# Kernel tuning notes

Measured on AMD Instinct MI355X. Metric: run time of the kernel, lower is better.

## Reference

```python
import jax, jax.numpy as jnp
import numpy as np

NUM_HEADS = 12

def _pe(L, d):
    # standard sinusoidal positional encoding, shape (1, L, d)
    pos = jnp.arange(L, dtype=jnp.float32)[:, None]
    i = jnp.arange(d)[None, :]
    angle = pos / jnp.power(10000.0, (2 * (i // 2)).astype(jnp.float32) / d)
    pe = jnp.where(i % 2 == 0, jnp.sin(angle), jnp.cos(angle))
    return pe[None]

def _ln(x, scale, bias, eps=1e-5):
    m = x.mean(-1, keepdims=True)
    v = ((x - m) ** 2).mean(-1, keepdims=True)
    return (x - m) / jnp.sqrt(v + eps) * scale + bias

def setup_inputs() -> dict:
    key = jax.random.key(0)
    ks = jax.random.split(key, 8)
    D = 768
    s = 0.02
    return {
        "x": jax.random.normal(ks[0], (8, D, 32, 32), jnp.float32),
        "context_token": jax.random.normal(ks[1], (1, 1, D), jnp.float32),
        "register_tokens": jax.random.normal(ks[2], (1, 4, D), jnp.float32),
        "in_proj_w": jax.random.normal(ks[3], (3 * D, D), jnp.float32) * s,
        "in_proj_b": jnp.zeros((3 * D,), jnp.float32),
        "out_proj_w": jax.random.normal(ks[4], (D, D), jnp.float32) * s,
        "out_proj_b": jnp.zeros((D,), jnp.float32),
        "ln1_s": jnp.ones((D,), jnp.float32),
        "ln1_b": jnp.zeros((D,), jnp.float32),
        "ln2_s": jnp.ones((D,), jnp.float32),
        "ln2_b": jnp.zeros((D,), jnp.float32),
        "ffn_w1": jax.random.normal(ks[5], (4 * D, D), jnp.float32) * s,
        "ffn_b1": jnp.zeros((4 * D,), jnp.float32),
        "ffn_w2": jax.random.normal(ks[6], (D, 4 * D), jnp.float32) * s,
        "ffn_b2": jnp.zeros((D,), jnp.float32),
    }

def reference(x, context_token, register_tokens, in_proj_w, in_proj_b,
              out_proj_w, out_proj_b, ln1_s, ln1_b, ln2_s, ln2_b,
              ffn_w1, ffn_b1, ffn_w2, ffn_b2):
    B, d, h, w = x.shape
    N = h * w
    R = register_tokens.shape[1]
    G = 1 + R  # global tokens: context + registers
    nh = NUM_HEADS
    dh = d // nh
    # (B, N, d)
    x_flat = x.reshape(B, d, N).transpose(0, 2, 1)
    tokens = jnp.concatenate([
        jnp.broadcast_to(context_token, (B, 1, d)),
        jnp.broadcast_to(register_tokens, (B, R, d)),
    ], axis=1)
    tokens = tokens + _pe(G, d)
    xwt = _ln(jnp.concatenate([tokens, x_flat], axis=1), ln1_s, ln1_b)
    S = G + N
    # MultiheadAttention (eval mode, dropout off): fused in-projection
    qkv = xwt @ in_proj_w.T + in_proj_b
    q, k, v = jnp.split(qkv, 3, axis=-1)
    to_heads = lambda t: t.reshape(B, S, nh, dh).transpose(0, 2, 1, 3)
    q, k, v = to_heads(q), to_heads(k), to_heads(v)
    scores = jnp.einsum('bhqd,bhkd->bhqk', q, k) / np.float32(np.sqrt(dh))
    # mask (True = disallowed): feature rows (>=G) cannot attend to global cols (<G);
    # global rows attend everything; feature-feature block allowed.
    row_feat = jnp.arange(S) >= G
    col_glob = jnp.arange(S) < G
    disallowed = row_feat[:, None] & col_glob[None, :]
    scores = jnp.where(disallowed, -jnp.inf, scores)
    attn = jax.nn.softmax(scores, axis=-1)
    o = jnp.einsum('bhqk,bhkd->bhqd', attn, v).transpose(0, 2, 1, 3).reshape(B, S, d)
    o = o @ out_proj_w.T + out_proj_b
    y = o + xwt
    ff = jax.nn.gelu(_ln(y, ln2_s, ln2_b) @ ffn_w1.T + ffn_b1, approximate=False) @ ffn_w2.T + ffn_b2
    y = y + ff
    context_out = y[:, 0:1, :]
    register_out = y[:, 1:G, :]
    feature_out = y[:, G:, :].transpose(0, 2, 1).reshape(B, d, h, w)
    return feature_out, context_out, register_out
```

## Files before the change

### kernel.cpp

```cpp
#include <hip/hip_runtime.h>
#include <hip/hip_bf16.h>
#include <cmath>

typedef unsigned short u16;
typedef __bf16 bf16x8 __attribute__((ext_vector_type(8)));
typedef float floatx4 __attribute__((ext_vector_type(4)));

#define SQ 1029
#define DM 768
#define NH 12
#define SQP 1088
#define SSC 0.18033688011112042f

#define GLD16(gp, lp) __builtin_amdgcn_global_load_lds( \
    (const __attribute__((address_space(1))) unsigned int*)(gp), \
    (__attribute__((address_space(3))) unsigned int*)(lp), 16, 0, 0)

#define OFF_WQKV ((size_t)0)
#define OFF_WOUT ((size_t)3538944)
#define OFF_W1   ((size_t)4718592)
#define OFF_W2   ((size_t)9437184)
#define OFF_XF   ((size_t)14155776)
#define OFF_XWT  ((size_t)26800128)
#define OFF_QKV  ((size_t)39444480)
#define OFF_VT   ((size_t)77783040)
#define OFF_Y    ((size_t)91152384)
#define OFF_BQ   ((size_t)103796736)

__device__ __forceinline__ float bf2f(u16 u) {
  unsigned int x = ((unsigned int)u) << 16;
  float f; __builtin_memcpy(&f, &x, 4); return f;
}
__device__ __forceinline__ u16 f2bf(float f) {
  unsigned int x; __builtin_memcpy(&x, &f, 4);
  x = (x + 0x7fffu + ((x >> 16) & 1u)) >> 16;
  return (u16)x;
}
__device__ __forceinline__ unsigned int pk_bf16(float a, float b) {
  __hip_bfloat162 h = __float22bfloat162_rn(make_float2(a, b));
  unsigned int u; __builtin_memcpy(&u, &h, 4); return u;
}

__device__ __forceinline__ void blockReduce2(float& s1, float& s2) {
  #pragma unroll
  for (int o = 32; o > 0; o >>= 1) { s1 += __shfl_xor(s1, o); s2 += __shfl_xor(s2, o); }
  __shared__ float t1[4], t2[4];
  const int w = threadIdx.x >> 6;
  if ((threadIdx.x & 63) == 0) { t1[w] = s1; t2[w] = s2; }
  __syncthreads();
  s1 = t1[0] + t1[1] + t1[2] + t1[3];
  s2 = t2[0] + t2[1] + t2[2] + t2[3];
}

__global__ __launch_bounds__(256) void convw_all(
    const float* __restrict__ a, const float* __restrict__ b,
    const float* __restrict__ c, const float* __restrict__ d,
    const float* __restrict__ bq, u16* __restrict__ dst, float* __restrict__ bqs) {
  int i = blockIdx.x * 256 + threadIdx.x;
  if (i >= 1770048) return;
  if (i >= 1769472) {
    const int off = i - 1769472;
    float4 v = ((const float4*)bq)[off];
    if (off < 192) { v.x *= SSC; v.y *= SSC; v.z *= SSC; v.w *= SSC; }
    ((float4*)bqs)[off] = v;
    return;
  }
  const float* src; int off;
  if (i < 442368)       { src = a; off = i; }
  else if (i < 589824)  { src = b; off = i - 442368; }
  else if (i < 1179648) { src = c; off = i - 589824; }
  else                  { src = d; off = i - 1179648; }
  float4 v = ((const float4*)src)[off];
  if (i < 147456) { v.x *= SSC; v.y *= SSC; v.z *= SSC; v.w *= SSC; }
  ushort4 o; o.x = f2bf(v.x); o.y = f2bf(v.y); o.z = f2bf(v.z); o.w = f2bf(v.w);
  ((ushort4*)dst)[i] = o;
}

__global__ __launch_bounds__(256) void ln1_fused(
    const float* __restrict__ x, const float* __restrict__ ctx, const float* __restrict__ regt,
    const float* __restrict__ g, const float* __restrict__ be, u16* __restrict__ xwt) {
  const int bx = blockIdx.x;
  const int tid = threadIdx.x;
  if (bx >= 256) {
    const int row = bx - 256;
    const int b = row / 5, s = row % 5;
    float v[3];
    #pragma unroll
    for (int i = 0; i < 3; ++i) {
      const int c = tid + i * 256;
      float tok = (s == 0) ? ctx[c] : regt[(s - 1) * DM + c];
      float e = (float)(2 * (c / 2)) * (1.0f / 768.0f);
      float ang = (float)s / powf(10000.0f, e);
      v[i] = tok + ((c & 1) ? cosf(ang) : sinf(ang));
    }
    float s1 = v[0] + v[1] + v[2];
    float s2 = v[0] * v[0] + v[1] * v[1] + v[2] * v[2];
    blockReduce2(s1, s2);
    const float mean = s1 * (1.0f / 768.0f);
    const float var = s2 * (1.0f / 768.0f) - mean * mean;
    const float rs = rsqrtf(fmaxf(var, 0.0f) + 1e-5f);
    #pragma unroll
    for (int i = 0; i < 3; ++i) {
      const int c = tid + i * 256;
      xwt[((size_t)b * SQ + s) * DM + c] = f2bf((v[i] - mean) * rs * g[c] + be[c]);
    }
    return;
  }
  __shared__ u16 XT[32][772];
  const int b = bx >> 5, st = bx & 31;
  const int i2 = tid & 15, cj = tid >> 4;
  const int n0 = st * 32;
  #pragma unroll 4
  for (int ct = 0; ct < 48; ++ct) {
    const int c = ct * 16 + cj;
    const float2 v = *(const float2*)&x[((size_t)b * 768 + c) * 1024 + n0 + i2 * 2];
    XT[i2 * 2][c]     = f2bf(v.x);
    XT[i2 * 2 + 1][c] = f2bf(v.y);
  }
  __syncthreads();
  const int wave = tid >> 6, lane = tid & 63;
  float gr[12], br[12];
  #pragma unroll
  for (int k = 0; k < 12; ++k) { gr[k] = g[lane + k * 64]; br[k] = be[lane + k * 64]; }
  #pragma unroll
  for (int rr = 0; rr < 8; ++rr) {
    const int row = wave * 8 + rr;
    float v[12];
    float s1 = 0.f, s2 = 0.f;
    #pragma unroll
    for (int k = 0; k < 12; ++k) {
      v[k] = bf2f(XT[row][lane + k * 64]);
      s1 += v[k]; s2 += v[k] * v[k];
    }
    #pragma unroll
    for (int o = 32; o > 0; o >>= 1) { s1 += __shfl_xor(s1, o); s2 += __shfl_xor(s2, o); }
    const float mean = s1 * (1.0f / 768.0f);
    const float var = s2 * (1.0f / 768.0f) - mean * mean;
    const float rs = rsqrtf(fmaxf(var, 0.0f) + 1e-5f);
    u16* dst = xwt + ((size_t)b * SQ + 5 + n0 + row) * DM;
    #pragma unroll
    for (int k = 0; k < 12; ++k)
      dst[lane + k * 64] = f2bf((v[k] - mean) * rs * gr[k] + br[k]);
  }
}

__global__ __launch_bounds__(256) void ln2k(
    const u16* __restrict__ y, const float* __restrict__ g, const float* __restrict__ be,
    u16* __restrict__ out) {
  const int row = blockIdx.x * 4 + (threadIdx.x >> 6);
  const int lane = threadIdx.x & 63;
  const u16* src = y + (size_t)row * DM;
  float v[12];
  float s1 = 0.f, s2 = 0.f;
  #pragma unroll
  for (int k = 0; k < 3; ++k) {
    const ushort4 u = *(const ushort4*)&src[k * 256 + lane * 4];
    const float a0 = bf2f(u.x), a1 = bf2f(u.y), a2 = bf2f(u.z), a3 = bf2f(u.w);
    v[k * 4 + 0] = a0; v[k * 4 + 1] = a1; v[k * 4 + 2] = a2; v[k * 4 + 3] = a3;
    s1 += (a0 + a1) + (a2 + a3);
    s2 += (a0 * a0 + a1 * a1) + (a2 * a2 + a3 * a3);
  }
  #pragma unroll
  for (int o = 32; o > 0; o >>= 1) { s1 += __shfl_xor(s1, o); s2 += __shfl_xor(s2, o); }
  const float mean = s1 * (1.0f / 768.0f);
  const float var = s2 * (1.0f / 768.0f) - mean * mean;
  const float rs = rsqrtf(fmaxf(var, 0.0f) + 1e-5f);
  u16* dst = out + (size_t)row * DM;
  #pragma unroll
  for (int k = 0; k < 3; ++k) {
    const float4 g4 = *(const float4*)&g[k * 256 + lane * 4];
    const float4 b4 = *(const float4*)&be[k * 256 + lane * 4];
    uint2 w;
    w.x = pk_bf16((v[k * 4 + 0] - mean) * rs * g4.x + b4.x,
                  (v[k * 4 + 1] - mean) * rs * g4.y + b4.y);
    w.y = pk_bf16((v[k * 4 + 2] - mean) * rs * g4.z + b4.z,
                  (v[k * 4 + 3] - mean) * rs * g4.w + b4.w);
    *(uint2*)&dst[k * 256 + lane * 4] = w;
  }
}

template<int EPI, int K, int NB>
__global__ __launch_bounds__(256) void gemmk(
    const u16* __restrict__ A, const u16* __restrict__ W, const float* __restrict__ bias,
    const u16* __restrict__ res, u16* __restrict__ out, int M) {
  constexpr int N = NB * 128;
  __shared__ u16 SM[16384];
  u16* Asm = SM;
  u16* Bsm = SM + 8192;
  const int tid = threadIdx.x, wave = tid >> 6, lane = tid & 63, quad = lane >> 4, l16 = lane & 15;
  const int lin = blockIdx.x;
  constexpr int FULL = 64 * NB;
  int mb, nb;
  if (lin < FULL) { const int g = lin / (8 * NB); const int r = lin - g * 8 * NB; mb = g * 8 + (r & 7); nb = r >> 3; }
  else { mb = 64; nb = lin - FULL; }
  const int m0 = mb * 128, n0 = nb * 128;
  const int wm = wave & 1, wn = wave >> 1;

  const u16* Ap[4]; const u16* Wp[4]; u16* la[4]; u16* lb[4];
  #pragma unroll
  for (int it = 0; it < 4; ++it) {
    const int c = it * 256 + tid;
    const int row = c >> 3, gch = (c & 7) ^ (row & 7);
    Ap[it] = A + (size_t)min(m0 + row, M - 1) * K + gch * 8;
    Wp[it] = W + (size_t)(n0 + row) * K + gch * 8;
    la[it] = Asm + c * 8;
    lb[it] = Bsm + c * 8;
  }

  floatx4 acc[4][4];
  #pragma unroll
  for (int i = 0; i < 4; ++i)
    #pragma unroll
    for (int j = 0; j < 4; ++j) { floatx4 z = {0.f, 0.f, 0.f, 0.f}; acc[i][j] = z; }

  const int ch0 = (quad ^ (l16 & 7)) << 3;
  const int ch1 = ((4 + quad) ^ (l16 & 7)) << 3;

  #pragma unroll 1
  for (int ko = 0; ko < K / 768; ++ko) {
    #pragma unroll
    for (int ki = 0; ki < 768; ki += 64) {
      __syncthreads();
      #pragma unroll
      for (int it = 0; it < 4; ++it) GLD16(Ap[it] + ki, la[it]);
      #pragma unroll
      for (int it = 0; it < 4; ++it) GLD16(Wp[it] + ki, lb[it]);
      __syncthreads();
      #pragma unroll
      for (int kk = 0; kk < 2; ++kk) {
        const int ch = kk ? ch1 : ch0;
        bf16x8 a[4], b[4];
        #pragma unroll
        for (int i = 0; i < 4; ++i) a[i] = *(const bf16x8*)&Asm[(wm * 64 + i * 16 + l16) * 64 + ch];
        #pragma unroll
        for (int j = 0; j < 4; ++j) b[j] = *(const bf16x8*)&Bsm[(wn * 64 + j * 16 + l16) * 64 + ch];
        #pragma unroll
        for (int i = 0; i < 4; ++i)
          #pragma unroll
          for (int j = 0; j < 4; ++j)
            acc[i][j] = __builtin_amdgcn_mfma_f32_16x16x32_bf16(b[j], a[i], acc[i][j], 0, 0, 0);
      }
    }
    if (K > 768) {
      #pragma unroll
      for (int it = 0; it < 4; ++it) { Ap[it] += 768; Wp[it] += 768; }
    }
  }

  #pragma unroll
  for (int j = 0; j < 4; ++j) {
    const float4 b4 = *(const float4*)(bias + n0 + wn * 64 + j * 16 + quad * 4);
    #pragma unroll
    for (int i = 0; i < 4; ++i) {
      acc[i][j][0] += b4.x; acc[i][j][1] += b4.y; acc[i][j][2] += b4.z; acc[i][j][3] += b4.w;
    }
  }
  if constexpr (EPI == 2) {
    #pragma unroll
    for (int i = 0; i < 4; ++i)
      #pragma unroll
      for (int j = 0; j < 4; ++j)
        #pragma unroll
        for (int r = 0; r < 4; ++r) {
          const float v = acc[i][j][r];
          acc[i][j][r] = v / (1.0f + exp2f(-2.3022221f * (v + 0.044715f * v * v * v)));
        }
  }
  __syncthreads();
  u16* Ep = SM + wave * 2304;
  #pragma unroll
  for (int h = 0; h < 2; ++h) {
    #pragma unroll
    for (int i2 = 0; i2 < 2; ++i2) {
      const int i = h * 2 + i2;
      #pragma unroll
      for (int j = 0; j < 4; ++j) {
        uint2 w;
        w.x = pk_bf16(acc[i][j][0], acc[i][j][1]);
        w.y = pk_bf16(acc[i][j][2], acc[i][j][3]);
        *(uint2*)&Ep[(i2 * 16 + l16) * 72 + j * 16 + quad * 4] = w;
      }
    }
    #pragma unroll
    for (int s = 0; s < 4; ++s) {
      const int lrow = s * 8 + (lane >> 3);
      const int gm = m0 + wm * 64 + h * 32 + lrow;
      const int gn = n0 + wn * 64 + (lane & 7) * 8;
      uint4 lv = *(const uint4*)&Ep[lrow * 72 + (lane & 7) * 8];
      if constexpr (EPI == 1 || EPI == 3) {
        const uint4 rv = *(const uint4*)(res + (size_t)min(gm, M - 1) * N + gn);
        const unsigned* lp = &lv.x; const unsigned* rp = &rv.x;
        uint4 ov; unsigned* op = &ov.x;
        #pragma unroll
        for (int d = 0; d < 4; ++d) {
          const float a0 = bf2f((u16)(lp[d] & 0xffffu)) + bf2f((u16)(rp[d] & 0xffffu));
          const float a1 = bf2f((u16)(lp[d] >> 16)) + bf2f((u16)(rp[d] >> 16));
          op[d] = pk_bf16(a0, a1);
        }
        lv = ov;
      }
      if (gm < M) *(uint4*)(out + (size_t)gm * N + gn) = lv;
    }
  }
}

template<int EPI, int K, int NB>
__global__ __launch_bounds__(128, 2) void gemmw(
    const u16* __restrict__ A, const u16* __restrict__ W, const float* __restrict__ bias,
    const u16* __restrict__ res, u16* __restrict__ out, int M) {
  constexpr int N = NB * 128;
  __shared__ u16 SM[16384];
  u16* Asm = SM;
  u16* Bsm = SM + 8192;
  const int tid = threadIdx.x, wave = tid >> 6, lane = tid & 63, quad = lane >> 4, l16 = lane & 15;
  const int lin = blockIdx.x;
  constexpr int FULL = 64 * NB;
  int mb, nb;
  if (lin < FULL) { const int g = lin / (8 * NB); const int r = lin - g * 8 * NB; mb = g * 8 + (r & 7); nb = r >> 3; }
  else { mb = 64; nb = lin - FULL; }
  const int m0 = mb * 128, n0 = nb * 128;

  const u16* Ap[8]; const u16* Wp[8];
  #pragma unroll
  for (int it = 0; it < 8; ++it) {
    const int row = it * 16 + (tid >> 3);
    const int gch = (tid & 7) ^ (row & 7);
    Ap[it] = A + (size_t)min(m0 + row, M - 1) * K + gch * 8;
    Wp[it] = W + (size_t)(n0 + row) * K + gch * 8;
  }

  floatx4 acc[8][4];
  #pragma unroll
  for (int i = 0; i < 8; ++i)
    #pragma unroll
    for (int j = 0; j < 4; ++j) { floatx4 z = {0.f, 0.f, 0.f, 0.f}; acc[i][j] = z; }

  const int ch0 = (quad ^ (l16 & 7)) << 3;
  const int ch1 = ((4 + quad) ^ (l16 & 7)) << 3;

  #pragma unroll 1
  for (int ko = 0; ko < K / 768; ++ko) {
    #pragma unroll
    for (int ki = 0; ki < 768; ki += 64) {
      __syncthreads();
      #pragma unroll
      for (int it = 0; it < 8; ++it) GLD16(Ap[it] + ki, (char*)SM + (it * 128 + tid) * 16);
      #pragma unroll
      for (int it = 0; it < 8; ++it) GLD16(Wp[it] + ki, (char*)SM + 16384 + (it * 128 + tid) * 16);
      __syncthreads();
      #pragma unroll
      for (int kk = 0; kk < 2; ++kk) {
        const int ch = kk ? ch1 : ch0;
        bf16x8 a[8], b[4];
        #pragma unroll
        for (int i = 0; i < 8; ++i) a[i] = *(const bf16x8*)&Asm[(i * 16 + l16) * 64 + ch];
        #pragma unroll
        for (int j = 0; j < 4; ++j) b[j] = *(const bf16x8*)&Bsm[(wave * 64 + j * 16 + l16) * 64 + ch];
        #pragma unroll
        for (int i = 0; i < 8; ++i)
          #pragma unroll
          for (int j = 0; j < 4; ++j)
            acc[i][j] = __builtin_amdgcn_mfma_f32_16x16x32_bf16(b[j], a[i], acc[i][j], 0, 0, 0);
      }
    }
    if (K > 768) {
      #pragma unroll
      for (int it = 0; it < 8; ++it) { Ap[it] += 768; Wp[it] += 768; }
    }
  }

  #pragma unroll
  for (int j = 0; j < 4; ++j) {
    const float4 b4 = *(const float4*)(bias + n0 + wave * 64 + j * 16 + quad * 4);
    #pragma unroll
    for (int i = 0; i < 8; ++i) {
      acc[i][j][0] += b4.x; acc[i][j][1] += b4.y; acc[i][j][2] += b4.z; acc[i][j][3] += b4.w;
    }
  }
  if constexpr (EPI == 2) {
    #pragma unroll
    for (int i = 0; i < 8; ++i)
      #pragma unroll
      for (int j = 0; j < 4; ++j)
        #pragma unroll
        for (int r = 0; r < 4; ++r) {
          const float v = acc[i][j][r];
          acc[i][j][r] = v / (1.0f + exp2f(-2.3022221f * (v + 0.044715f * v * v * v)));
        }
  }
  __syncthreads();
  u16* Ep = SM + wave * 2304;
  #pragma unroll
  for (int g = 0; g < 4; ++g) {
    #pragma unroll
    for (int i2 = 0; i2 < 2; ++i2) {
      const int i = g * 2 + i2;
      #pragma unroll
      for (int j = 0; j < 4; ++j) {
        uint2 w;
        w.x = pk_bf16(acc[i][j][0], acc[i][j][1]);
        w.y = pk_bf16(acc[i][j][2], acc[i][j][3]);
        *(uint2*)&Ep[(i2 * 16 + l16) * 72 + j * 16 + quad * 4] = w;
      }
    }
    #pragma unroll
    for (int s = 0; s < 4; ++s) {
      const int lrow = s * 8 + (lane >> 3);
      const int gm = m0 + g * 32 + lrow;
      const int gn = n0 + wave * 64 + (lane & 7) * 8;
      uint4 lv = *(const uint4*)&Ep[lrow * 72 + (lane & 7) * 8];
      if constexpr (EPI == 1 || EPI == 3) {
        const uint4 rv = *(const uint4*)(res + (size_t)min(gm, M - 1) * N + gn);
        const unsigned* lp = &lv.x; const unsigned* rp = &rv.x;
        uint4 ov; unsigned* op = &ov.x;
        #pragma unroll
        for (int d = 0; d < 4; ++d) {
          const float a0 = bf2f((u16)(lp[d] & 0xffffu)) + bf2f((u16)(rp[d] & 0xffffu));
          const float a1 = bf2f((u16)(lp[d] >> 16)) + bf2f((u16)(rp[d] >> 16));
          op[d] = pk_bf16(a0, a1);
        }
        lv = ov;
      }
      if (gm < M) *(uint4*)(out + (size_t)gm * N + gn) = lv;
    }
  }
}

__global__ __launch_bounds__(256) void vtrans(const u16* __restrict__ qkv, u16* __restrict__ vt) {
  __shared__ u16 t[32][33];
  const int bh = blockIdx.x, st = blockIdx.y, dt = blockIdx.z;
  const int bq = bh / NH, hh = bh % NH;
  u16* vd = vt + (size_t)bh * 64 * SQP;
  const int i = threadIdx.x, jj = threadIdx.y;
  #pragma unroll
  for (int kk = 0; kk < 4; ++kk) {
    int j = jj + kk * 8;
    t[j][i] = qkv[(size_t)(bq * SQ + st * 32 + j) * 2304 + 1536 + hh * 64 + dt * 32 + i];
  }
  __syncthreads();
  #pragma unroll
  for (int kk = 0; kk < 4; ++kk) {
    int j = jj + kk * 8;
    vd[(size_t)(dt * 32 + j) * SQP + st * 32 + i] = t[i][j];
  }
}

__global__ __launch_bounds__(256) void attn_flash(
    const u16* __restrict__ qkv, const u16* __restrict__ vt, u16* __restrict__ out) {
  const int bh = blockIdx.x, qt = blockIdx.y;
  const int b = bh / NH, h = bh % NH;
  const int tid = threadIdx.x, wave = tid >> 6, lane = tid & 63, quad = lane >> 4, l16 = lane & 15;
  __shared__ u16 Ks[4096], VTs[4096];
  __shared__ u16 Ps[64 * 72];
  const int q0 = qt * 64;
  const u16* qk = qkv + (size_t)b * SQ * 2304 + h * 64;
  const u16* vslab = vt + (size_t)bh * 64 * SQP;
  const int r0 = tid >> 3,         q0c = (tid & 7) ^ (r0 & 7);
  const int r1 = (tid + 256) >> 3, q1c = (tid & 7) ^ (r1 & 7);
  u16* L0K = Ks + wave * 512;  u16* L1K = Ks + 2048 + wave * 512;
  u16* L0V = VTs + wave * 512; u16* L1V = VTs + 2048 + wave * 512;

  const int qrow = wave * 16 + l16;
  const bf16x8 qf0 = *(const bf16x8*)&qk[(size_t)(q0 + qrow) * 2304 + quad * 8];
  const bf16x8 qf1 = *(const bf16x8*)&qk[(size_t)(q0 + qrow) * 2304 + (4 + quad) * 8];

  floatx4 Oa[4];
  #pragma unroll
  for (int nt = 0; nt < 4; ++nt) { floatx4 z = {0.f, 0.f, 0.f, 0.f}; Oa[nt] = z; }
  float l_acc = 0.f;
  const bool qfeat = (q0 + qrow >= 5);

  for (int t = 0; t < 17; ++t) {
    const int k0 = t * 64;
    __syncthreads();
    GLD16(qk + 768 + (size_t)(k0 + r0) * 2304 + q0c * 8, L0K);
    GLD16(qk + 768 + (size_t)(k0 + r1) * 2304 + q1c * 8, L1K);
    GLD16(vslab + (size_t)r0 * SQP + k0 + q0c * 8, L0V);
    GLD16(vslab + (size_t)r1 * SQP + k0 + q1c * 8, L1V);
    __syncthreads();

    floatx4 st[4];
    #pragma unroll
    for (int mt = 0; mt < 4; ++mt) { floatx4 z = {0.f, 0.f, 0.f, 0.f}; st[mt] = z; }
    #pragma unroll
    for (int kk = 0; kk < 2; ++kk) {
      const bf16x8 qf = kk ? qf1 : qf0;
      #pragma unroll
      for (int mt = 0; mt < 4; ++mt) {
        const int krow = mt * 16 + l16;
        bf16x8 kf = *(const bf16x8*)&Ks[krow * 64 + (((kk * 4 + quad) ^ (krow & 7)) << 3)];
        st[mt] = __builtin_amdgcn_mfma_f32_16x16x32_bf16(kf, qf, st[mt], 0, 0, 0);
      }
    }

    if (t == 16) {
      float p[4];
      #pragma unroll
      for (int r = 0; r < 4; ++r) {
        float pv = exp2f(st[0][r]);
        p[r] = (quad * 4 + r < 5) ? pv : 0.f;
      }
      l_acc += (p[0] + p[1]) + (p[2] + p[3]);
      uint2 w;
      w.x = pk_bf16(p[0], p[1]);
      w.y = pk_bf16(p[2], p[3]);
      *(uint2*)&Ps[qrow * 72 + quad * 4] = w;
      const uint2 zz = {0u, 0u};
      #pragma unroll
      for (int mt = 1; mt < 4; ++mt) *(uint2*)&Ps[qrow * 72 + mt * 16 + quad * 4] = zz;
    } else if (t == 0) {
      #pragma unroll
      for (int mt = 0; mt < 4; ++mt) {
        float p[4];
        #pragma unroll
        for (int r = 0; r < 4; ++r) {
          float pv = exp2f(st[mt][r]);
          if (mt == 0) pv = (qfeat && (quad * 4 + r < 5)) ? 0.f : pv;
          p[r] = pv;
        }
        l_acc += (p[0] + p[1]) + (p[2] + p[3]);
        uint2 w;
        w.x = pk_bf16(p[0], p[1]);
        w.y = pk_bf16(p[2], p[3]);
        *(uint2*)&Ps[qrow * 72 + mt * 16 + quad * 4] = w;
      }
    } else {
      #pragma unroll
      for (int mt = 0; mt < 4; ++mt) {
        float p[4];
        #pragma unroll
        for (int r = 0; r < 4; ++r) p[r] = exp2f(st[mt][r]);
        l_acc += (p[0] + p[1]) + (p[2] + p[3]);
        uint2 w;
        w.x = pk_bf16(p[0], p[1]);
        w.y = pk_bf16(p[2], p[3]);
        *(uint2*)&Ps[qrow * 72 + mt * 16 + quad * 4] = w;
      }
    }

    auto pv_step = [&](int kk) {
      bf16x8 pf = *(const bf16x8*)&Ps[qrow * 72 + kk * 32 + quad * 8];
      #pragma unroll
      for (int nt = 0; nt < 4; ++nt) {
        const int brow = nt * 16 + l16;
        bf16x8 bb = *(const bf16x8*)&VTs[brow * 64 + (((kk * 4 + quad) ^ (brow & 7)) << 3)];
        Oa[nt] = __builtin_amdgcn_mfma_f32_16x16x32_bf16(pf, bb, Oa[nt], 0, 0, 0);
      }
    };
    pv_step(0);
    if (t != 16) pv_step(1);
  }

  float lt = l_acc;
  lt += __shfl_xor(lt, 16);
  lt += __shfl_xor(lt, 32);
  lt = fmaxf(lt, 1e-30f);
  #pragma unroll
  for (int nt = 0; nt < 4; ++nt)
    #pragma unroll
    for (int r = 0; r < 4; ++r) {
      const int qo = quad * 4 + r;
      const float lr = __shfl(lt, (lane & 48) | qo);
      const int qg2 = q0 + wave * 16 + qo;
      if (qg2 < SQ)
        out[((size_t)b * SQ + qg2) * DM + h * 64 + nt * 16 + l16] = f2bf(Oa[nt][r] / lr);
    }
}

__global__ __launch_bounds__(256) void transpose_out(const u16* __restrict__ yf, float* __restrict__ out) {
  const int bx = blockIdx.x;
  const int tid = threadIdx.x;
  if (bx >= 6144) {
    const int idx = (bx - 6144) * 256 + tid;
    if (idx >= 8 * 5 * DM) return;
    const int b = idx / (5 * DM);
    const int r = idx % (5 * DM);
    const int s = r / DM, c = r % DM;
    const float v = bf2f(yf[((size_t)b * SQ + s) * DM + c]);
    if (s == 0) out[(size_t)6291456 + (size_t)b * DM + c] = v;
    else out[(size_t)6291456 + 6144 + ((size_t)b * 4 + (s - 1)) * DM + c] = v;
    return;
  }
  __shared__ u16 tile[32][33];
  const int b = bx / 768, rr = bx % 768, nt = rr / 24, ct = rr % 24;
  const int i = tid & 31, jj = tid >> 5;
  #pragma unroll
  for (int kk = 0; kk < 4; ++kk) {
    int j = jj + kk * 8;
    tile[j][i] = yf[((size_t)b * SQ + 5 + nt * 32 + j) * DM + ct * 32 + i];
  }
  __syncthreads();
  #pragma unroll
  for (int kk = 0; kk < 4; ++kk) {
    int j = jj + kk * 8;
    out[((size_t)b * 768 + ct * 32 + j) * 1024 + nt * 32 + i] = bf2f(tile[i][j]);
  }
}

extern "C" void kernel_launch(void* const* d_in, const int* in_sizes, int n_in,
                              void* d_out, int out_size, void* d_ws, size_t ws_size,
                              hipStream_t stream) {
  const float* x    = (const float*)d_in[0];
  const float* ctx  = (const float*)d_in[1];
  const float* regt = (const float*)d_in[2];
  const float* wqkv = (const float*)d_in[3];
  const float* bqkv = (const float*)d_in[4];
  const float* wout = (const float*)d_in[5];
  const float* bout = (const float*)d_in[6];
  const float* ln1s = (const float*)d_in[7];
  const float* ln1b = (const float*)d_in[8];
  const float* ln2s = (const float*)d_in[9];
  const float* ln2b = (const float*)d_in[10];
  const float* w1   = (const float*)d_in[11];
  const float* b1   = (const float*)d_in[12];
  const float* w2   = (const float*)d_in[13];
  const float* b2   = (const float*)d_in[14];

  char* ws = (char*)d_ws;
  u16* wb_all = (u16*)(ws + OFF_WQKV);
  u16* wqkv_b = (u16*)(ws + OFF_WQKV);
  u16* wout_b = (u16*)(ws + OFF_WOUT);
  u16* w1_b   = (u16*)(ws + OFF_W1);
  u16* w2_b   = (u16*)(ws + OFF_W2);
  u16* xwt    = (u16*)(ws + OFF_XWT);
  u16* qkv    = (u16*)(ws + OFF_QKV);
  u16* vtb    = (u16*)(ws + OFF_VT);
  u16* yb     = (u16*)(ws + OFF_Y);
  float* bqs  = (float*)(ws + OFF_BQ);
  u16* attnb  = (u16*)(ws + OFF_XF);
  u16* ynorm  = (u16*)(ws + OFF_XF);
  u16* h1     = (u16*)(ws + OFF_QKV);
  u16* yfin   = (u16*)(ws + OFF_XWT);
  float* outp = (float*)d_out;

  convw_all   <<<6915, 256, 0, stream>>>(wqkv, wout, w1, w2, bqkv, wb_all, bqs);
  ln1_fused   <<<296, 256, 0, stream>>>(x, ctx, regt, ln1s, ln1b, xwt);
  gemmw<0, 768, 18><<<65 * 18, 128, 0, stream>>>(xwt, wqkv_b, bqs, nullptr, qkv, 8232);
  vtrans      <<<dim3(96, 34, 2), dim3(32, 8), 0, stream>>>(qkv, vtb);
  attn_flash  <<<dim3(96, 17), 256, 0, stream>>>(qkv, vtb, attnb);
  gemmk<1, 768, 6><<<65 * 6, 256, 0, stream>>>(attnb, wout_b, bout, xwt, yb, 8232);
  ln2k        <<<2058, 256, 0, stream>>>(yb, ln2s, ln2b, ynorm);
  gemmk<2, 768, 24><<<65 * 24, 256, 0, stream>>>(ynorm, w1_b, b1, nullptr, h1, 8232);
  gemmk<3, 3072, 6><<<65 * 6, 256, 0, stream>>>(h1, w2_b, b2, yb, yfin, 8232);
  transpose_out<<<6264, 256, 0, stream>>>(yfin, outp);
}
```

Baseline: 385.9 us.

## Fuse V transpose into QKV GEMM epilogue and output transpose into FFN2 epilogue

The QKV GEMM epilogue now writes the V columns transposed straight into the vt buffer, which removes the separate vtrans kernel. A small vt_zero kernel clears the padded tail. The final FFN GEMM epilogue writes the feature output directly in the channel-major fp32 image layout, which replaces the big transpose_out kernel with a small one that handles only the global tokens. Both changes save a full read and write of large intermediates, at the cost of strided scalar global stores in the epilogues. Unused EPI branches in gemmw were also pruned.

```diff
diff --git a/kernel.cpp b/kernel.cpp
--- a/kernel.cpp
+++ b/kernel.cpp
@@ -76,6 +76,14 @@
   ((ushort4*)dst)[i] = o;
 }
 
+__global__ __launch_bounds__(256) void vt_zero(u16* __restrict__ vt) {
+  const int i = blockIdx.x * 256 + threadIdx.x;
+  if (i >= 49152) return;
+  const int seg = i >> 2, part = i & 3;
+  const uint4 z = {0u, 0u, 0u, 0u};
+  *(uint4*)&vt[(size_t)seg * SQP + 1024 + part * 8] = z;
+}
+
 __global__ __launch_bounds__(256) void ln1_fused(
     const float* __restrict__ x, const float* __restrict__ ctx, const float* __restrict__ regt,
     const float* __restrict__ g, const float* __restrict__ be, u16* __restrict__ xwt) {
@@ -182,7 +190,7 @@
 template<int EPI, int K, int NB>
 __global__ __launch_bounds__(256) void gemmk(
     const u16* __restrict__ A, const u16* __restrict__ W, const float* __restrict__ bias,
-    const u16* __restrict__ res, u16* __restrict__ out, int M) {
+    const u16* __restrict__ res, u16* __restrict__ out, float* __restrict__ oimg, int M) {
   constexpr int N = NB * 128;
   __shared__ u16 SM[16384];
   u16* Asm = SM;
@@ -298,8 +306,22 @@
           op[d] = pk_bf16(a0, a1);
         }
         lv = ov;
+        if constexpr (EPI == 3)
+          *(uint4*)&Ep[lrow * 72 + (lane & 7) * 8] = lv;
       }
       if (gm < M) *(uint4*)(out + (size_t)gm * N + gn) = lv;
+    }
+    if constexpr (EPI == 3) {
+      const int sloc = lane & 31, chi = lane >> 5;
+      const int gm2 = m0 + wm * 64 + h * 32 + sloc;
+      const int bb = gm2 / SQ;
+      const int srow = gm2 - bb * SQ;
+      if (gm2 < M && srow >= 5) {
+        float* od = oimg + ((size_t)bb * 768 + n0 + wn * 64 + chi) * 1024 + (srow - 5);
+        #pragma unroll
+        for (int cc = 0; cc < 64; cc += 2)
+          od[(size_t)cc * 1024] = bf2f(Ep[sloc * 72 + cc + chi]);
+      }
     }
   }
 }
@@ -307,7 +329,7 @@
 template<int EPI, int K, int NB>
 __global__ __launch_bounds__(128, 2) void gemmw(
     const u16* __restrict__ A, const u16* __restrict__ W, const float* __restrict__ bias,
-    const u16* __restrict__ res, u16* __restrict__ out, int M) {
+    const u16* __restrict__ res, u16* __restrict__ out, u16* __restrict__ vt, int M) {
   constexpr int N = NB * 128;
   __shared__ u16 SM[16384];
   u16* Asm = SM;
@@ -377,17 +399,6 @@
       acc[i][j][0] += b4.x; acc[i][j][1] += b4.y; acc[i][j][2] += b4.z; acc[i][j][3] += b4.w;
     }
   }
-  if constexpr (EPI == 2) {
-    #pragma unroll
-    for (int i = 0; i < 8; ++i)
-      #pragma unroll
-      for (int j = 0; j < 4; ++j)
-        #pragma unroll
-        for (int r = 0; r < 4; ++r) {
-          const float v = acc[i][j][r];
-          acc[i][j][r] = v / (1.0f + exp2f(-2.3022221f * (v + 0.044715f * v * v * v)));
-        }
-  }
   __syncthreads();
   u16* Ep = SM + wave * 2304;
   #pragma unroll
@@ -409,39 +420,24 @@
       const int gm = m0 + g * 32 + lrow;
       const int gn = n0 + wave * 64 + (lane & 7) * 8;
       uint4 lv = *(const uint4*)&Ep[lrow * 72 + (lane & 7) * 8];
-      if constexpr (EPI == 1 || EPI == 3) {
-        const uint4 rv = *(const uint4*)(res + (size_t)min(gm, M - 1) * N + gn);
-        const unsigned* lp = &lv.x; const unsigned* rp = &rv.x;
-        uint4 ov; unsigned* op = &ov.x;
-        #pragma unroll
-        for (int d = 0; d < 4; ++d) {
-          const float a0 = bf2f((u16)(lp[d] & 0xffffu)) + bf2f((u16)(rp[d] & 0xffffu));
-          const float a1 = bf2f((u16)(lp[d] >> 16)) + bf2f((u16)(rp[d] >> 16));
-          op[d] = pk_bf16(a0, a1);
+      if (gm < M) *(uint4*)(out + (size_t)gm * N + gn) = lv;
+    }
+    if constexpr (EPI == 0) {
+      const int vcol0 = n0 + wave * 64;
+      if (vcol0 >= 1536) {
+        const int hh = (vcol0 - 1536) >> 6;
+        const int sloc = lane & 31, dhi = lane >> 5;
+        const int gm2 = m0 + g * 32 + sloc;
+        const int bb = gm2 / SQ;
+        const int ss = gm2 - bb * SQ;
+        if (gm2 < M) {
+          u16* vdst = vt + (((size_t)bb * NH + hh) * 64 + dhi) * SQP + ss;
+          #pragma unroll
+          for (int dd = 0; dd < 64; dd += 2)
+            vdst[(size_t)dd * SQP] = Ep[sloc * 72 + dd + dhi];
         }
-        lv = ov;
-      }
-      if (gm < M) *(uint4*)(out + (size_t)gm * N + gn) = lv;
-    }
-  }
-}
-
-__global__ __launch_bounds__(256) void vtrans(const u16* __restrict__ qkv, u16* __restrict__ vt) {
-  __shared__ u16 t[32][33];
-  const int bh = blockIdx.x, st = blockIdx.y, dt = blockIdx.z;
-  const int bq = bh / NH, hh = bh % NH;
-  u16* vd = vt + (size_t)bh * 64 * SQP;
-  const int i = threadIdx.x, jj = threadIdx.y;
-  #pragma unroll
-  for (int kk = 0; kk < 4; ++kk) {
-    int j = jj + kk * 8;
-    t[j][i] = qkv[(size_t)(bq * SQ + st * 32 + j) * 2304 + 1536 + hh * 64 + dt * 32 + i];
-  }
-  __syncthreads();
-  #pragma unroll
-  for (int kk = 0; kk < 4; ++kk) {
-    int j = jj + kk * 8;
-    vd[(size_t)(dt * 32 + j) * SQP + st * 32 + i] = t[i][j];
+      }
+    }
   }
 }
 
@@ -567,34 +563,15 @@
     }
 }
 
-__global__ __launch_bounds__(256) void transpose_out(const u16* __restrict__ yf, float* __restrict__ out) {
-  const int bx = blockIdx.x;
-  const int tid = threadIdx.x;
-  if (bx >= 6144) {
-    const int idx = (bx - 6144) * 256 + tid;
-    if (idx >= 8 * 5 * DM) return;
-    const int b = idx / (5 * DM);
-    const int r = idx % (5 * DM);
-    const int s = r / DM, c = r % DM;
-    const float v = bf2f(yf[((size_t)b * SQ + s) * DM + c]);
-    if (s == 0) out[(size_t)6291456 + (size_t)b * DM + c] = v;
-    else out[(size_t)6291456 + 6144 + ((size_t)b * 4 + (s - 1)) * DM + c] = v;
-    return;
-  }
-  __shared__ u16 tile[32][33];
-  const int b = bx / 768, rr = bx % 768, nt = rr / 24, ct = rr % 24;
-  const int i = tid & 31, jj = tid >> 5;
-  #pragma unroll
-  for (int kk = 0; kk < 4; ++kk) {
-    int j = jj + kk * 8;
-    tile[j][i] = yf[((size_t)b * SQ + 5 + nt * 32 + j) * DM + ct * 32 + i];
-  }
-  __syncthreads();
-  #pragma unroll
-  for (int kk = 0; kk < 4; ++kk) {
-    int j = jj + kk * 8;
-    out[((size_t)b * 768 + ct * 32 + j) * 1024 + nt * 32 + i] = bf2f(tile[i][j]);
-  }
+__global__ __launch_bounds__(256) void out_small(const u16* __restrict__ yf, float* __restrict__ out) {
+  const int idx = blockIdx.x * 256 + threadIdx.x;
+  if (idx >= 8 * 5 * DM) return;
+  const int b = idx / (5 * DM);
+  const int r = idx % (5 * DM);
+  const int s = r / DM, c = r % DM;
+  const float v = bf2f(yf[((size_t)b * SQ + s) * DM + c]);
+  if (s == 0) out[(size_t)6291456 + (size_t)b * DM + c] = v;
+  else out[(size_t)6291456 + 6144 + ((size_t)b * 4 + (s - 1)) * DM + c] = v;
 }
 
 extern "C" void kernel_launch(void* const* d_in, const int* in_sizes, int n_in,
@@ -634,13 +611,13 @@
   float* outp = (float*)d_out;
 
   convw_all   <<<6915, 256, 0, stream>>>(wqkv, wout, w1, w2, bqkv, wb_all, bqs);
+  vt_zero     <<<192, 256, 0, stream>>>(vtb);
   ln1_fused   <<<296, 256, 0, stream>>>(x, ctx, regt, ln1s, ln1b, xwt);
-  gemmw<0, 768, 18><<<65 * 18, 128, 0, stream>>>(xwt, wqkv_b, bqs, nullptr, qkv, 8232);
-  vtrans      <<<dim3(96, 34, 2), dim3(32, 8), 0, stream>>>(qkv, vtb);
+  gemmw<0, 768, 18><<<65 * 18, 128, 0, stream>>>(xwt, wqkv_b, bqs, nullptr, qkv, vtb, 8232);
   attn_flash  <<<dim3(96, 17), 256, 0, stream>>>(qkv, vtb, attnb);
-  gemmk<1, 768, 6><<<65 * 6, 256, 0, stream>>>(attnb, wout_b, bout, xwt, yb, 8232);
+  gemmk<1, 768, 6><<<65 * 6, 256, 0, stream>>>(attnb, wout_b, bout, xwt, yb, nullptr, 8232);
   ln2k        <<<2058, 256, 0, stream>>>(yb, ln2s, ln2b, ynorm);
-  gemmk<2, 768, 24><<<65 * 24, 256, 0, stream>>>(ynorm, w1_b, b1, nullptr, h1, 8232);
-  gemmk<3, 3072, 6><<<65 * 6, 256, 0, stream>>>(h1, w2_b, b2, yb, yfin, 8232);
-  transpose_out<<<6264, 256, 0, stream>>>(yfin, outp);
-}
+  gemmk<2, 768, 24><<<65 * 24, 256, 0, stream>>>(ynorm, w1_b, b1, nullptr, h1, nullptr, 8232);
+  gemmk<3, 3072, 6><<<65 * 6, 256, 0, stream>>>(h1, w2_b, b2, yb, yfin, outp, 8232);
+  out_small   <<<120, 256, 0, stream>>>(yfin, outp);
+}
```

Result: no change. 387.5 us (+0.4%).
